# Kernel optimization log

Hardware: AMD Instinct MI355X
Metric: run time of the kernel (lower is better)

Reference implementation:

```python
import jax, jax.numpy as jnp
import numpy as np

HEAD_DIM = 128


def block_causal_mask(cu_seqlens, seq_len, dtype):
    # positions -> which packed document each token belongs to
    positions = jnp.arange(seq_len)
    seq_ids = jnp.searchsorted(cu_seqlens, positions, side='right') - 1
    same_seq = seq_ids[:, None] == seq_ids[None, :]
    causal = positions[None, :] <= positions[:, None]  # key_pos <= query_pos
    neg_inf = jnp.asarray(float('-inf'), dtype)
    return jnp.where(same_seq & causal, jnp.asarray(0.0, dtype), neg_inf)


def setup_inputs() -> dict:
    key = jax.random.key(0)
    kq, kk, kv = jax.random.split(key, 3)
    B, H, S, D = 1, 8, 4096, HEAD_DIM
    q = jax.random.normal(kq, (B, H, S, D), dtype=jnp.float32)
    k = jax.random.normal(kk, (B, H, S, D), dtype=jnp.float32)
    v = jax.random.normal(kv, (B, H, S, D), dtype=jnp.float32)
    # 4 packed documents of length 1024 each; cu_seqlens[-1] == seq_len
    cu_seqlens = jnp.array([0, 1024, 2048, 3072, 4096], dtype=jnp.int32)
    return {"q": q, "k": k, "v": v, "cu_seqlens": cu_seqlens, "max_seqlen": 1024}


def reference(q, k, v, cu_seqlens, max_seqlen):
    seq_len = q.shape[2]
    scale = 1.0 / jnp.sqrt(jnp.asarray(q.shape[-1], q.dtype))
    mask = block_causal_mask(cu_seqlens, seq_len, q.dtype)  # [S, S]
    # scores: [B, H, Sq, Sk]
    scores = jnp.einsum('bhqd,bhkd->bhqk', q, k) * scale + mask
    probs = jax.nn.softmax(scores, axis=-1)
    return jnp.einsum('bhqk,bhkd->bhqd', probs, v)
```

## Files before the change

### kernel.cpp

```cpp
#include <hip/hip_runtime.h>
#include <hip/hip_bf16.h>


#define HD 128
#define BR 64
#define BC 128

typedef __attribute__((ext_vector_type(8))) short short8;
typedef __attribute__((ext_vector_type(4))) float floatx4;

__device__ inline unsigned packbf2(float lo, float hi) {
    __hip_bfloat162 h2 = __float22bfloat162_rn(make_float2(lo, hi));
    return *reinterpret_cast<unsigned*>(&h2);
}
__device__ inline short bfs(float f) {
    __hip_bfloat16 b = __float2bfloat16(f);
    return *reinterpret_cast<short*>(&b);
}

__device__ inline void gll16(const void* g, void* l) {
    __builtin_amdgcn_global_load_lds(
        (const __attribute__((address_space(1))) unsigned int*)g,
        (__attribute__((address_space(3))) unsigned int*)l, 16, 0, 0);
}

__global__ __launch_bounds__(256) void prepack(
    const float* __restrict__ K, const float* __restrict__ V,
    unsigned short* __restrict__ wsK, unsigned short* __restrict__ wsVT,
    int S)
{
    const int tid = threadIdx.x;
    const int nVblk = 8 * (S >> 6);
    const int bid = blockIdx.x;
    if (bid < nVblk) {
        __shared__ __align__(8) unsigned short sV[HD * 68];
        const int ntile = S >> 6;
        const int h = bid / ntile;
        const int t = bid - h * ntile;
        const float* vb = V + ((size_t)h * S + t * 64) * HD;
        {
            const int rp = tid >> 3;
            const int dc = tid & 7;
            const int r0 = rp * 2;
            const int d0 = dc * 16;
            const float* p0 = vb + (size_t)r0 * HD + d0;
            const float* p1 = p0 + HD;
            float4 a0 = *(const float4*)(p0 + 0),  a1 = *(const float4*)(p0 + 4);
            float4 a2 = *(const float4*)(p0 + 8),  a3 = *(const float4*)(p0 + 12);
            float4 b0 = *(const float4*)(p1 + 0),  b1 = *(const float4*)(p1 + 4);
            float4 b2 = *(const float4*)(p1 + 8),  b3 = *(const float4*)(p1 + 12);
            float av[16] = {a0.x,a0.y,a0.z,a0.w, a1.x,a1.y,a1.z,a1.w,
                            a2.x,a2.y,a2.z,a2.w, a3.x,a3.y,a3.z,a3.w};
            float bv[16] = {b0.x,b0.y,b0.z,b0.w, b1.x,b1.y,b1.z,b1.w,
                            b2.x,b2.y,b2.z,b2.w, b3.x,b3.y,b3.z,b3.w};
            #pragma unroll
            for (int i = 0; i < 16; ++i) {
                unsigned pr = packbf2(av[i], bv[i]);
                *(unsigned*)((char*)sV + ((size_t)(d0 + i) * 68 + r0) * 2) = pr;
            }
        }
        __syncthreads();
        const int d  = tid >> 1;
        const int jj = tid & 1;
        char* dstrow = (char*)wsVT + (((size_t)(h * ntile + t) * HD + d) * 128);
        const int dx = (d & 7) << 4;
        const unsigned short* srow = sV + (size_t)d * 68;
        #pragma unroll
        for (int u = 0; u < 4; ++u) {
            const int j  = jj * 4 + u;
            const int k0 = (j >> 2) * 32 + (j & 3) * 4;
            uint2 lo = *(const uint2*)(srow + k0);
            uint2 hi = *(const uint2*)(srow + k0 + 16);
            uint4 w = make_uint4(lo.x, lo.y, hi.x, hi.y);
            *(uint4*)(dstrow + ((j * 16) ^ dx)) = w;
        }
    } else {
        const int cid = (bid - nVblk) * 256 + tid;
        const int row = cid >> 4;
        const int c   = cid & 15;
        const float* src = K + (size_t)row * HD + c * 8;
        float4 f0 = *(const float4*)src;
        float4 f1 = *(const float4*)(src + 4);
        union { uint4 q; unsigned u[4]; } w;
        w.u[0] = packbf2(f0.x, f0.y); w.u[1] = packbf2(f0.z, f0.w);
        w.u[2] = packbf2(f1.x, f1.y); w.u[3] = packbf2(f1.z, f1.w);
        *(uint4*)((char*)wsK + (size_t)row * 256 + ((c * 16) ^ ((row & 7) << 4))) = w.q;
    }
}

__global__ __launch_bounds__(512, 1) void fa_fwd(
    const float* __restrict__ Q,
    const unsigned short* __restrict__ wsK,
    const unsigned short* __restrict__ wsVT,
    const int* __restrict__ cu_seqlens, int n_cu,
    float* __restrict__ O,
    int S)
{
    __shared__ alignas(16) __hip_bfloat16 sK2[2][BC * HD];
    __shared__ alignas(16) unsigned int   sVT2[2][2 * HD * 32];

    const int tid  = threadIdx.x;
    const int wave = tid >> 6;
    const int gp   = wave >> 2;
    const int wsub = wave & 3;
    const int lane = tid & 63;
    const int quad = lane >> 4;
    const int l16  = lane & 15;
    const int kx   = (l16 & 7) << 4;

    const int nqb = S / BR;
    const int h   = blockIdx.x & 7;
    const int g   = (int)(blockIdx.x >> 3);
    int qb;
    if (nqb == 64) {
        qb = (g & 3) * 16 + (15 - (g >> 2));
    } else {
        qb = nqb - 1 - g;
    }
    const int q0    = qb * BR;
    const int qw    = q0 + wsub * 16;
    const int qlane = qw + l16;

    int blk_ds = 0;
    for (int i = 0; i < n_cu; ++i) {
        int c = cu_seqlens[i];
        if (c <= q0) blk_ds = c;
    }
    const int k_begin = blk_ds & ~(BC - 1);
    const int ntiles  = (q0 + BR - 1 - k_begin) / BC + 1;

    const char* gkb = (const char*)wsK + (size_t)h * S * 256;
    const char* gvb = (const char*)wsVT + (size_t)h * (S >> 6) * 16384;
    const int wofs = (wave & 3) * 8192;
    const int lo = wofs + lane * 16;
    auto stage = [&](int kt, int buf) {
        if (gp == 0) {
            const char* gk = gkb + (size_t)kt * 256 + lo;
            char* lk = (char*)&sK2[buf][0] + wofs;
            #pragma unroll
            for (int c = 0; c < 8; ++c) gll16(gk + c * 1024, lk + c * 1024);
        } else {
            const char* gv = gvb + (size_t)(kt >> 6) * 16384 + lo;
            char* lv = (char*)&sVT2[buf][0] + wofs;
            #pragma unroll
            for (int c = 0; c < 8; ++c) gll16(gv + c * 1024, lv + c * 1024);
        }
    };

    const size_t hoff = (size_t)h * S * HD;
    const float* Qh = Q + hoff;
    float*       Oh = O + hoff;

    short8 aq[4];
    {
        const float* qp = Qh + (size_t)qlane * HD + quad * 8;
        #pragma unroll
        for (int ks = 0; ks < 4; ++ks) {
            float4 a0 = *(const float4*)(qp + ks * 32);
            float4 a1 = *(const float4*)(qp + ks * 32 + 4);
            short8 a;
            a[0] = bfs(a0.x); a[1] = bfs(a0.y); a[2] = bfs(a0.z); a[3] = bfs(a0.w);
            a[4] = bfs(a1.x); a[5] = bfs(a1.y); a[6] = bfs(a1.z); a[7] = bfs(a1.w);
            aq[ks] = a;
        }
    }

    int ds_lane = 0;
    for (int i = 0; i < n_cu; ++i) {
        int c = cu_seqlens[i];
        if (c <= qlane) ds_lane = c;
    }

    stage(k_begin, 0);

    floatx4 oacc[8];
    #pragma unroll
    for (int dt = 0; dt < 8; ++dt) oacc[dt] = (floatx4){0.f, 0.f, 0.f, 0.f};
    float m_r = -1e30f, l_r = 0.f;

    const float sl = 0.08838834764831845f * 1.4426950408889634f;

    for (int it = 0; it < ntiles; ++it) {
        const int kt  = k_begin + it * BC;
        const int buf = it & 1;

        asm volatile("s_waitcnt vmcnt(0)\n\ts_barrier" ::: "memory");

        if (it + 1 < ntiles) stage(kt + BC, buf ^ 1);

        if (kt + gp * 64 <= qw + 15) {
            const char* kbase = (const char*)&sK2[buf][0];
            const char* vbase = (const char*)&sVT2[buf][0] + gp * 16384;

            floatx4 sc[4];
            __builtin_amdgcn_s_setprio(1);
            #pragma unroll
            for (int ctl = 0; ctl < 4; ++ctl) {
                if (kt + gp * 64 + ctl * 16 <= qw + 15) {
                    floatx4 c = (floatx4){0.f, 0.f, 0.f, 0.f};
                    #pragma unroll
                    for (int ks = 0; ks < 4; ++ks) {
                        short8 a = *(const short8*)(kbase
                            + (gp * 64 + ctl * 16 + l16) * 256
                            + (((ks * 4 + quad) << 4) ^ kx));
                        c = __builtin_amdgcn_mfma_f32_16x16x32_bf16(a, aq[ks], c, 0, 0, 0);
                    }
                    sc[ctl] = c;
                } else {
                    sc[ctl] = (floatx4){-1e30f, -1e30f, -1e30f, -1e30f};
                }
            }
            __builtin_amdgcn_s_setprio(0);

            #pragma unroll
            for (int ctl = 0; ctl < 4; ++ctl) {
                if (kt + gp * 64 + ctl * 16 <= qw + 15) {
                    #pragma unroll
                    for (int r = 0; r < 4; ++r) {
                        const int key = kt + gp * 64 + ctl * 16 + quad * 4 + r;
                        const bool valid = (key <= qlane) && (key >= ds_lane);
                        float s = sc[ctl][r] * sl;
                        sc[ctl][r] = valid ? s : -1e30f;
                    }
                }
            }

            float mx01 = fmaxf(fmaxf(fmaxf(sc[0][0], sc[0][1]), fmaxf(sc[0][2], sc[0][3])),
                               fmaxf(fmaxf(sc[1][0], sc[1][1]), fmaxf(sc[1][2], sc[1][3])));
            float mx23 = fmaxf(fmaxf(fmaxf(sc[2][0], sc[2][1]), fmaxf(sc[2][2], sc[2][3])),
                               fmaxf(fmaxf(sc[3][0], sc[3][1]), fmaxf(sc[3][2], sc[3][3])));
            float mx = fmaxf(mx01, mx23);
            mx = fmaxf(mx, __shfl_xor(mx, 16, 64));
            mx = fmaxf(mx, __shfl_xor(mx, 32, 64));

            if (__any(mx > m_r + 8.f)) {
                const float mnew = fmaxf(m_r, mx);
                const float al   = exp2f(m_r - mnew);
                m_r = mnew;
                l_r *= al;
                #pragma unroll
                for (int dt = 0; dt < 8; ++dt) {
                    #pragma unroll
                    for (int r = 0; r < 4; ++r)
                        oacc[dt][r] *= al;
                }
            }
            const float live = (m_r > -1e29f) ? 1.f : 0.f;

            float ssum = 0.f;
            #pragma unroll
            for (int ctl = 0; ctl < 4; ++ctl) {
                #pragma unroll
                for (int r = 0; r < 4; ++r) {
                    float p = exp2f(sc[ctl][r] - m_r) * live;
                    sc[ctl][r] = p;
                    ssum += p;
                }
            }
            l_r += ssum;

            __builtin_amdgcn_s_setprio(1);
            #pragma unroll
            for (int ks = 0; ks < 2; ++ks) {
                if (kt + gp * 64 + ks * 32 <= qw + 15) {
                    union { unsigned u[4]; short8 s; } pu;
                    pu.u[0] = packbf2(sc[2*ks][0],   sc[2*ks][1]);
                    pu.u[1] = packbf2(sc[2*ks][2],   sc[2*ks][3]);
                    pu.u[2] = packbf2(sc[2*ks+1][0], sc[2*ks+1][1]);
                    pu.u[3] = packbf2(sc[2*ks+1][2], sc[2*ks+1][3]);
                    #pragma unroll
                    for (int dt = 0; dt < 8; ++dt) {
                        union { uint4 q; short8 s; } cv;
                        cv.q = *(const uint4*)(vbase + (dt * 16 + l16) * 128
                                               + (((ks * 4 + quad) << 4) ^ kx));
                        oacc[dt] = __builtin_amdgcn_mfma_f32_16x16x32_bf16(cv.s, pu.s, oacc[dt], 0, 0, 0);
                    }
                }
            }
            __builtin_amdgcn_s_setprio(0);
        }
    }

    l_r += __shfl_xor(l_r, 16, 64);
    l_r += __shfl_xor(l_r, 32, 64);

    __syncthreads();

    float* obuf = (float*)&sK2[0][0];
    float* lbuf = (float*)&sVT2[0][0];
    if (gp == 1) {
        float* ob = obuf + wsub * 2048;
        #pragma unroll
        for (int dt = 0; dt < 8; ++dt) {
            const int sw = (dt ^ (lane & 7)) << 2;
            float4 st;
            st.x = oacc[dt][0]; st.y = oacc[dt][1];
            st.z = oacc[dt][2]; st.w = oacc[dt][3];
            *(float4*)(ob + lane * 32 + sw) = st;
        }
        if (quad == 0) {
            lbuf[wsub * 128 + l16]      = m_r;
            lbuf[wsub * 128 + 64 + l16] = l_r;
        }
    }
    __syncthreads();
    if (gp == 0) {
        const float m2 = lbuf[wsub * 128 + l16];
        const float l2 = lbuf[wsub * 128 + 64 + l16];
        const float M  = fmaxf(m_r, m2);
        const float w1 = exp2f(m_r - M);
        const float w2 = exp2f(m2 - M);
        const float inv = 1.0f / (w1 * l_r + w2 * l2);
        const float* ob = obuf + wsub * 2048;
        float* op = Oh + (size_t)qlane * HD + quad * 4;
        #pragma unroll
        for (int dt = 0; dt < 8; ++dt) {
            const int sw = (dt ^ (lane & 7)) << 2;
            float4 o2 = *(const float4*)(ob + lane * 32 + sw);
            float4 st;
            st.x = (w1 * oacc[dt][0] + w2 * o2.x) * inv;
            st.y = (w1 * oacc[dt][1] + w2 * o2.y) * inv;
            st.z = (w1 * oacc[dt][2] + w2 * o2.z) * inv;
            st.w = (w1 * oacc[dt][3] + w2 * o2.w) * inv;
            *(float4*)(op + dt * 16) = st;
        }
    }
}

extern "C" void kernel_launch(void* const* d_in, const int* in_sizes, int n_in,
                              void* d_out, int out_size, void* d_ws, size_t ws_size,
                              hipStream_t stream) {
    const float* q = (const float*)d_in[0];
    const float* k = (const float*)d_in[1];
    const float* v = (const float*)d_in[2];
    const int* cu = (const int*)d_in[3];
    const int n_cu = in_sizes[3];
    const int H = 8;
    const int S = in_sizes[0] / (H * HD);
    float* out = (float*)d_out;

    const int nqb = S / BR;
    unsigned short* wsK  = (unsigned short*)d_ws;
    unsigned short* wsVT = wsK + (size_t)H * S * HD;

    const int nVblk = H * (S >> 6);
    const int nKblk = (H * S) / 16;
    prepack<<<dim3(nVblk + nKblk), dim3(256), 0, stream>>>(k, v, wsK, wsVT, S);

    dim3 grid(H * nqb);
    dim3 block(512);
    fa_fwd<<<grid, block, 0, stream>>>(q, wsK, wsVT, cu, n_cu, out, S);
}
```

Before: 126.5 us.

## Read K and V tiles directly from global memory instead of LDS staging

```diff
diff --git a/kernel.cpp b/kernel.cpp
--- a/kernel.cpp
+++ b/kernel.cpp
@@ -17,12 +17,7 @@
     __hip_bfloat16 b = __float2bfloat16(f);
     return *reinterpret_cast<short*>(&b);
 }
-
-__device__ inline void gll16(const void* g, void* l) {
-    __builtin_amdgcn_global_load_lds(
-        (const __attribute__((address_space(1))) unsigned int*)g,
-        (__attribute__((address_space(3))) unsigned int*)l, 16, 0, 0);
-}
+__device__ inline float fexp2(float x) { return __builtin_amdgcn_exp2f(x); }
 
 __global__ __launch_bounds__(256) void prepack(
     const float* __restrict__ K, const float* __restrict__ V,
@@ -35,8 +30,8 @@
     if (bid < nVblk) {
         __shared__ __align__(8) unsigned short sV[HD * 68];
         const int ntile = S >> 6;
-        const int h = bid / ntile;
-        const int t = bid - h * ntile;
+        const int h = bid & 7;
+        const int t = bid >> 3;
         const float* vb = V + ((size_t)h * S + t * 64) * HD;
         {
             const int rp = tid >> 3;
@@ -63,7 +58,6 @@
         const int d  = tid >> 1;
         const int jj = tid & 1;
         char* dstrow = (char*)wsVT + (((size_t)(h * ntile + t) * HD + d) * 128);
-        const int dx = (d & 7) << 4;
         const unsigned short* srow = sV + (size_t)d * 68;
         #pragma unroll
         for (int u = 0; u < 4; ++u) {
@@ -72,23 +66,27 @@
             uint2 lo = *(const uint2*)(srow + k0);
             uint2 hi = *(const uint2*)(srow + k0 + 16);
             uint4 w = make_uint4(lo.x, lo.y, hi.x, hi.y);
-            *(uint4*)(dstrow + ((j * 16) ^ dx)) = w;
+            *(uint4*)(dstrow + j * 16) = w;
         }
     } else {
-        const int cid = (bid - nVblk) * 256 + tid;
-        const int row = cid >> 4;
-        const int c   = cid & 15;
-        const float* src = K + (size_t)row * HD + c * 8;
+        const int b2  = bid - nVblk;
+        const int h   = b2 & 7;
+        const int idx = b2 >> 3;
+        const int cid = idx * 256 + tid;
+        const int rowh = cid >> 4;
+        const int c    = cid & 15;
+        const size_t row = (size_t)h * S + rowh;
+        const float* src = K + row * HD + c * 8;
         float4 f0 = *(const float4*)src;
         float4 f1 = *(const float4*)(src + 4);
         union { uint4 q; unsigned u[4]; } w;
         w.u[0] = packbf2(f0.x, f0.y); w.u[1] = packbf2(f0.z, f0.w);
         w.u[2] = packbf2(f1.x, f1.y); w.u[3] = packbf2(f1.z, f1.w);
-        *(uint4*)((char*)wsK + (size_t)row * 256 + ((c * 16) ^ ((row & 7) << 4))) = w.q;
-    }
-}
-
-__global__ __launch_bounds__(512, 1) void fa_fwd(
+        *(uint4*)((char*)wsK + row * 256 + c * 16) = w.q;
+    }
+}
+
+__global__ __launch_bounds__(512, 4) void fa_fwd(
     const float* __restrict__ Q,
     const unsigned short* __restrict__ wsK,
     const unsigned short* __restrict__ wsVT,
@@ -96,8 +94,8 @@
     float* __restrict__ O,
     int S)
 {
-    __shared__ alignas(16) __hip_bfloat16 sK2[2][BC * HD];
-    __shared__ alignas(16) unsigned int   sVT2[2][2 * HD * 32];
+    __shared__ alignas(16) float obuf[4 * 2048];
+    __shared__ alignas(16) float lbuf[4 * 128];
 
     const int tid  = threadIdx.x;
     const int wave = tid >> 6;
@@ -106,17 +104,13 @@
     const int lane = tid & 63;
     const int quad = lane >> 4;
     const int l16  = lane & 15;
-    const int kx   = (l16 & 7) << 4;
 
     const int nqb = S / BR;
     const int h   = blockIdx.x & 7;
     const int g   = (int)(blockIdx.x >> 3);
     int qb;
-    if (nqb == 64) {
-        qb = (g & 3) * 16 + (15 - (g >> 2));
-    } else {
-        qb = nqb - 1 - g;
-    }
+    if (nqb == 64) qb = (g & 3) * 16 + (15 - (g >> 2));
+    else           qb = nqb - 1 - g;
     const int q0    = qb * BR;
     const int qw    = q0 + wsub * 16;
     const int qlane = qw + l16;
@@ -131,21 +125,6 @@
 
     const char* gkb = (const char*)wsK + (size_t)h * S * 256;
     const char* gvb = (const char*)wsVT + (size_t)h * (S >> 6) * 16384;
-    const int wofs = (wave & 3) * 8192;
-    const int lo = wofs + lane * 16;
-    auto stage = [&](int kt, int buf) {
-        if (gp == 0) {
-            const char* gk = gkb + (size_t)kt * 256 + lo;
-            char* lk = (char*)&sK2[buf][0] + wofs;
-            #pragma unroll
-            for (int c = 0; c < 8; ++c) gll16(gk + c * 1024, lk + c * 1024);
-        } else {
-            const char* gv = gvb + (size_t)(kt >> 6) * 16384 + lo;
-            char* lv = (char*)&sVT2[buf][0] + wofs;
-            #pragma unroll
-            for (int c = 0; c < 8; ++c) gll16(gv + c * 1024, lv + c * 1024);
-        }
-    };
 
     const size_t hoff = (size_t)h * S * HD;
     const float* Qh = Q + hoff;
@@ -171,8 +150,6 @@
         if (c <= qlane) ds_lane = c;
     }
 
-    stage(k_begin, 0);
-
     floatx4 oacc[8];
     #pragma unroll
     for (int dt = 0; dt < 8; ++dt) oacc[dt] = (floatx4){0.f, 0.f, 0.f, 0.f};
@@ -181,113 +158,104 @@
     const float sl = 0.08838834764831845f * 1.4426950408889634f;
 
     for (int it = 0; it < ntiles; ++it) {
-        const int kt  = k_begin + it * BC;
-        const int buf = it & 1;
-
-        asm volatile("s_waitcnt vmcnt(0)\n\ts_barrier" ::: "memory");
-
-        if (it + 1 < ntiles) stage(kt + BC, buf ^ 1);
-
-        if (kt + gp * 64 <= qw + 15) {
-            const char* kbase = (const char*)&sK2[buf][0];
-            const char* vbase = (const char*)&sVT2[buf][0] + gp * 16384;
-
-            floatx4 sc[4];
-            __builtin_amdgcn_s_setprio(1);
+        const int kt = k_begin + it * BC;
+        if (kt + gp * 64 > qw + 15) continue;
+
+        const char* ktb = gkb + (size_t)(kt + gp * 64) * 256;
+        const char* vtb = gvb + (size_t)((kt >> 6) + gp) * 16384;
+
+        floatx4 sc[4];
+        __builtin_amdgcn_s_setprio(1);
+        #pragma unroll
+        for (int ctl = 0; ctl < 4; ++ctl) {
+            if (kt + gp * 64 + ctl * 16 <= qw + 15) {
+                short8 a[4];
+                #pragma unroll
+                for (int ks = 0; ks < 4; ++ks)
+                    a[ks] = *(const short8*)(ktb + (ctl * 16 + l16) * 256
+                                             + (ks * 4 + quad) * 16);
+                floatx4 c = (floatx4){0.f, 0.f, 0.f, 0.f};
+                #pragma unroll
+                for (int ks = 0; ks < 4; ++ks)
+                    c = __builtin_amdgcn_mfma_f32_16x16x32_bf16(a[ks], aq[ks], c, 0, 0, 0);
+                sc[ctl] = c;
+            } else {
+                sc[ctl] = (floatx4){-1e30f, -1e30f, -1e30f, -1e30f};
+            }
+        }
+        __builtin_amdgcn_s_setprio(0);
+
+        #pragma unroll
+        for (int ctl = 0; ctl < 4; ++ctl) {
+            if (kt + gp * 64 + ctl * 16 <= qw + 15) {
+                #pragma unroll
+                for (int r = 0; r < 4; ++r) {
+                    const int key = kt + gp * 64 + ctl * 16 + quad * 4 + r;
+                    const bool valid = (key <= qlane) && (key >= ds_lane);
+                    float s = sc[ctl][r] * sl;
+                    sc[ctl][r] = valid ? s : -1e30f;
+                }
+            }
+        }
+
+        float mx01 = fmaxf(fmaxf(fmaxf(sc[0][0], sc[0][1]), fmaxf(sc[0][2], sc[0][3])),
+                           fmaxf(fmaxf(sc[1][0], sc[1][1]), fmaxf(sc[1][2], sc[1][3])));
+        float mx23 = fmaxf(fmaxf(fmaxf(sc[2][0], sc[2][1]), fmaxf(sc[2][2], sc[2][3])),
+                           fmaxf(fmaxf(sc[3][0], sc[3][1]), fmaxf(sc[3][2], sc[3][3])));
+        float mx = fmaxf(mx01, mx23);
+        mx = fmaxf(mx, __shfl_xor(mx, 16, 64));
+        mx = fmaxf(mx, __shfl_xor(mx, 32, 64));
+
+        if (__any(mx > m_r + 8.f)) {
+            const float mnew = fmaxf(m_r, mx);
+            const float al   = fexp2(m_r - mnew);
+            m_r = mnew;
+            l_r *= al;
             #pragma unroll
-            for (int ctl = 0; ctl < 4; ++ctl) {
-                if (kt + gp * 64 + ctl * 16 <= qw + 15) {
-                    floatx4 c = (floatx4){0.f, 0.f, 0.f, 0.f};
-                    #pragma unroll
-                    for (int ks = 0; ks < 4; ++ks) {
-                        short8 a = *(const short8*)(kbase
-                            + (gp * 64 + ctl * 16 + l16) * 256
-                            + (((ks * 4 + quad) << 4) ^ kx));
-                        c = __builtin_amdgcn_mfma_f32_16x16x32_bf16(a, aq[ks], c, 0, 0, 0);
-                    }
-                    sc[ctl] = c;
-                } else {
-                    sc[ctl] = (floatx4){-1e30f, -1e30f, -1e30f, -1e30f};
+            for (int dt = 0; dt < 8; ++dt) {
+                #pragma unroll
+                for (int r = 0; r < 4; ++r)
+                    oacc[dt][r] *= al;
+            }
+        }
+        const float live = (m_r > -1e29f) ? 1.f : 0.f;
+
+        float ssum = 0.f;
+        #pragma unroll
+        for (int ctl = 0; ctl < 4; ++ctl) {
+            #pragma unroll
+            for (int r = 0; r < 4; ++r) {
+                float p = fexp2(sc[ctl][r] - m_r) * live;
+                sc[ctl][r] = p;
+                ssum += p;
+            }
+        }
+        l_r += ssum;
+
+        __builtin_amdgcn_s_setprio(1);
+        #pragma unroll
+        for (int ks = 0; ks < 2; ++ks) {
+            if (kt + gp * 64 + ks * 32 <= qw + 15) {
+                union { unsigned u[4]; short8 s; } pu;
+                pu.u[0] = packbf2(sc[2*ks][0],   sc[2*ks][1]);
+                pu.u[1] = packbf2(sc[2*ks][2],   sc[2*ks][3]);
+                pu.u[2] = packbf2(sc[2*ks+1][0], sc[2*ks+1][1]);
+                pu.u[3] = packbf2(sc[2*ks+1][2], sc[2*ks+1][3]);
+                #pragma unroll
+                for (int dt = 0; dt < 8; ++dt) {
+                    union { uint4 q; short8 s; } cv;
+                    cv.q = *(const uint4*)(vtb + (dt * 16 + l16) * 128
+                                           + (ks * 4 + quad) * 16);
+                    oacc[dt] = __builtin_amdgcn_mfma_f32_16x16x32_bf16(cv.s, pu.s, oacc[dt], 0, 0, 0);
                 }
             }
-            __builtin_amdgcn_s_setprio(0);
-
-            #pragma unroll
-            for (int ctl = 0; ctl < 4; ++ctl) {
-                if (kt + gp * 64 + ctl * 16 <= qw + 15) {
-                    #pragma unroll
-                    for (int r = 0; r < 4; ++r) {
-                        const int key = kt + gp * 64 + ctl * 16 + quad * 4 + r;
-                        const bool valid = (key <= qlane) && (key >= ds_lane);
-                        float s = sc[ctl][r] * sl;
-                        sc[ctl][r] = valid ? s : -1e30f;
-                    }
-                }
-            }
-
-            float mx01 = fmaxf(fmaxf(fmaxf(sc[0][0], sc[0][1]), fmaxf(sc[0][2], sc[0][3])),
-                               fmaxf(fmaxf(sc[1][0], sc[1][1]), fmaxf(sc[1][2], sc[1][3])));
-            float mx23 = fmaxf(fmaxf(fmaxf(sc[2][0], sc[2][1]), fmaxf(sc[2][2], sc[2][3])),
-                               fmaxf(fmaxf(sc[3][0], sc[3][1]), fmaxf(sc[3][2], sc[3][3])));
-            float mx = fmaxf(mx01, mx23);
-            mx = fmaxf(mx, __shfl_xor(mx, 16, 64));
-            mx = fmaxf(mx, __shfl_xor(mx, 32, 64));
-
-            if (__any(mx > m_r + 8.f)) {
-                const float mnew = fmaxf(m_r, mx);
-                const float al   = exp2f(m_r - mnew);
-                m_r = mnew;
-                l_r *= al;
-                #pragma unroll
-                for (int dt = 0; dt < 8; ++dt) {
-                    #pragma unroll
-                    for (int r = 0; r < 4; ++r)
-                        oacc[dt][r] *= al;
-                }
-            }
-            const float live = (m_r > -1e29f) ? 1.f : 0.f;
-
-            float ssum = 0.f;
-            #pragma unroll
-            for (int ctl = 0; ctl < 4; ++ctl) {
-                #pragma unroll
-                for (int r = 0; r < 4; ++r) {
-                    float p = exp2f(sc[ctl][r] - m_r) * live;
-                    sc[ctl][r] = p;
-                    ssum += p;
-                }
-            }
-            l_r += ssum;
-
-            __builtin_amdgcn_s_setprio(1);
-            #pragma unroll
-            for (int ks = 0; ks < 2; ++ks) {
-                if (kt + gp * 64 + ks * 32 <= qw + 15) {
-                    union { unsigned u[4]; short8 s; } pu;
-                    pu.u[0] = packbf2(sc[2*ks][0],   sc[2*ks][1]);
-                    pu.u[1] = packbf2(sc[2*ks][2],   sc[2*ks][3]);
-                    pu.u[2] = packbf2(sc[2*ks+1][0], sc[2*ks+1][1]);
-                    pu.u[3] = packbf2(sc[2*ks+1][2], sc[2*ks+1][3]);
-                    #pragma unroll
-                    for (int dt = 0; dt < 8; ++dt) {
-                        union { uint4 q; short8 s; } cv;
-                        cv.q = *(const uint4*)(vbase + (dt * 16 + l16) * 128
-                                               + (((ks * 4 + quad) << 4) ^ kx));
-                        oacc[dt] = __builtin_amdgcn_mfma_f32_16x16x32_bf16(cv.s, pu.s, oacc[dt], 0, 0, 0);
-                    }
-                }
-            }
-            __builtin_amdgcn_s_setprio(0);
-        }
+        }
+        __builtin_amdgcn_s_setprio(0);
     }
 
     l_r += __shfl_xor(l_r, 16, 64);
     l_r += __shfl_xor(l_r, 32, 64);
 
-    __syncthreads();
-
-    float* obuf = (float*)&sK2[0][0];
-    float* lbuf = (float*)&sVT2[0][0];
     if (gp == 1) {
         float* ob = obuf + wsub * 2048;
         #pragma unroll
@@ -308,8 +276,8 @@
         const float m2 = lbuf[wsub * 128 + l16];
         const float l2 = lbuf[wsub * 128 + 64 + l16];
         const float M  = fmaxf(m_r, m2);
-        const float w1 = exp2f(m_r - M);
-        const float w2 = exp2f(m2 - M);
+        const float w1 = fexp2(m_r - M);
+        const float w2 = fexp2(m2 - M);
         const float inv = 1.0f / (w1 * l_r + w2 * l2);
         const float* ob = obuf + wsub * 2048;
         float* op = Oh + (size_t)qlane * HD + quad * 4;
```

Result: slower. 185.4 us (+46.6%).
